# Optimization experiments

Hardware: AMD Instinct MI355X
Metric: run time of the kernel (lower is better)

Reference implementation:

```python
import jax, jax.numpy as jnp
import numpy as np
jax.config.update("jax_enable_x64", True)  # hashing uses int64 primes as in torch

N_PTS = 1048576
L, T, F = 16, 2 ** 18, 2
N_MIN, N_MAX = 16, 1024
HID, OUT = 64, 3


def setup_inputs() -> dict:
    key = jax.random.key(0)
    ks = jax.random.split(key, 6)
    X = jax.random.uniform(ks[0], (N_PTS, 2), dtype=jnp.float32)
    hash_table = jax.random.uniform(ks[1], (L, T, F), dtype=jnp.float32,
                                    minval=-1e-4, maxval=1e-4)
    def lin(k, fan_in, fan_out):
        bound = 1.0 / np.sqrt(fan_in)
        kw, kb = jax.random.split(k)
        W = jax.random.uniform(kw, (fan_in, fan_out), dtype=jnp.float32,
                               minval=-bound, maxval=bound)
        b = jax.random.uniform(kb, (fan_out,), dtype=jnp.float32,
                               minval=-bound, maxval=bound)
        return W, b
    W1, b1 = lin(ks[2], L * F, HID)
    W2, b2 = lin(ks[3], HID, HID)
    W3, b3 = lin(ks[4], HID, HID)
    W4, b4 = lin(ks[5], HID, OUT)
    return {"X": X, "hash_table": hash_table,
            "W1": W1, "b1": b1, "W2": W2, "b2": b2,
            "W3": W3, "b3": b3, "W4": W4, "b4": b4}


def reference(X, hash_table, W1, b1, W2, b2, W3, b3, W4, b4):
    Lh, Th, Fh = hash_table.shape
    # per-level resolutions: floor(N_min * b**l), b geometric between N_min and N_max
    b_geo = np.exp((np.log(N_MAX) - np.log(N_MIN)) / (Lh - 1))
    N_values = jnp.floor(jnp.asarray(N_MIN * b_geo ** np.arange(Lh),
                                     dtype=jnp.float32))  # (L,)

    x_scaled = X[:, :, None] * N_values[None, None, :]        # (N, 2, L)
    x_floor = jnp.floor(x_scaled)

    # NOTE: original code MULTIPLIES floor coords by the 0/1 vertex pattern
    # (not add) -- we replicate that math faithfully.
    vertices = jnp.array([[0., 0., 1., 1.], [0., 1., 0., 1.]],
                         dtype=jnp.float32)                   # (2, 4)
    x_vert = (x_floor[:, :, :, None] * vertices[None, :, None, :]
              ).astype(jnp.int64)                             # (N, 2, L, 4)

    primes = jnp.array([1, 2654435761], dtype=jnp.int64)
    hv = x_vert * primes[None, :, None, None]
    x_hash = jnp.remainder(jnp.bitwise_xor(hv[:, 0], hv[:, 1]), Th)  # (N, L, 4)

    # irregular gather: per-level hash table lookup -> (N, L, 4, F)
    lookup = hash_table[jnp.arange(Lh)[None, :, None], x_hash]

    w = x_scaled - x_floor                                    # (N, 2, L)
    fx, fy = w[:, 0, :], w[:, 1, :]
    cx, cy = 1.0 - fx, 1.0 - fy
    f_stack = jnp.stack([cx * cy, cx * fy, fx * cy, fx * fy], axis=2)  # (N, L, 4)

    x_interp = jnp.sum(f_stack[:, :, :, None] * lookup, axis=2)  # (N, L, F)
    feat = x_interp.reshape(-1, Lh * Fh).astype(jnp.float32)     # (N, 32)

    h = jax.nn.leaky_relu(feat @ W1 + b1)
    h = jax.nn.leaky_relu(h @ W2 + b2)
    h = jax.nn.leaky_relu(h @ W3 + b3)
    return jax.nn.relu(h @ W4 + b4)
```

## Files before the change

kernel.cpp:

```cpp
#include <hip/hip_runtime.h>
#include <math.h>

typedef _Float16 half8  __attribute__((ext_vector_type(8)));
typedef float    float4v __attribute__((ext_vector_type(4)));

constexpr int T_ = 1 << 18;
constexpr unsigned TMASK = T_ - 1;
constexpr unsigned PRIME = 2654435761u;

constexpr int WFRAG_HALFS = 22 * 64 * 8;
constexpr int BIAS_FLOATS = 208;
constexpr int WS_BYTES    = 22528 + 240 * 4;
constexpr int WS_UINT4    = WS_BYTES / 16;
constexpr int V12_OFF     = 23488;

constexpr int BLK   = 256;
constexpr int PTS_PER_BLOCK = 512;

struct Meta { float n[16]; float off[16]; };

__global__ void prep_weights(const float* __restrict__ W1, const float* __restrict__ b1,
                             const float* __restrict__ W2, const float* __restrict__ b2,
                             const float* __restrict__ W3, const float* __restrict__ b3,
                             const float* __restrict__ W4, const float* __restrict__ b4,
                             const float2* __restrict__ table,
                             _Float16* __restrict__ wsW, float* __restrict__ wsB,
                             uint2* __restrict__ wsV, Meta mv)
{
    const int tid = threadIdx.x;
    const int bid = blockIdx.x;
    if (bid < 44) {
        const int e = bid * 256 + tid;
        const int frag = e >> 9;
        const int l    = (e >> 3) & 63;
        const int j    = e & 7;
        const int g = l >> 4, m = l & 15;
        const int u = j >> 2, r = j & 3;
        float v;
        if (frag < 4) {
            v = W1[(8*g + j) * 64 + 16*frag + m];
        } else if (frag < 12) {
            const int s = (frag - 4) >> 2, t = (frag - 4) & 3;
            v = W2[(32*s + 16*u + 4*g + r) * 64 + 16*t + m];
        } else if (frag < 20) {
            const int s = (frag - 12) >> 2, t = (frag - 12) & 3;
            v = W3[(32*s + 16*u + 4*g + r) * 64 + 16*t + m];
        } else {
            const int s = frag - 20;
            v = (m < 3) ? W4[(32*s + 16*u + 4*g + r) * 3 + m] : 0.f;
        }
        wsW[e] = (_Float16)v;
    } else if (bid == 44) {
        if (tid < 64) { wsB[tid] = b1[tid]; wsB[64 + tid] = b2[tid]; wsB[128 + tid] = b3[tid]; }
        else if (tid < 80)  { const int r2 = tid - 64; wsB[192 + r2] = (r2 < 3) ? b4[r2] : 0.f; }
        else if (tid < 96)  wsB[BIAS_FLOATS + (tid - 80)] = mv.n[tid - 80];
        else if (tid < 112) wsB[BIAS_FLOATS + 16 + (tid - 96)] = mv.off[tid - 96];
    } else {
        const int e = (bid - 45) * 256 + tid;
        const int total = (int)mv.off[15] + (int)mv.n[15] + 1;
        if (e < total) {
            int l = 0;
            #pragma unroll
            for (int k = 1; k < 16; ++k) if (e >= (int)mv.off[k]) l = k;
            const int i = e - (int)mv.off[l];
            const float2* tl = table + (size_t)l * T_;
            const float2 b = tl[((unsigned)i * PRIME) & TMASK];
            const float2 a = tl[i];
            union { _Float16 h[2]; unsigned u; } p0, p1;
            p0.h[0] = (_Float16)b.x; p0.h[1] = (_Float16)b.y;
            p1.h[0] = (_Float16)a.x; p1.h[1] = (_Float16)a.y;
            wsV[e] = uint2{p0.u, p1.u};
        }
    }
}

struct Gather {
    float2   v3[4];
    unsigned v1[4];
    unsigned v2[4];
};

__device__ __forceinline__ void issue_gather(Gather& G, const float2 xy,
                                             const float2* __restrict__ table,
                                             const unsigned* __restrict__ gV12,
                                             const float (&nvq)[4], const int (&offq)[4],
                                             const int g)
{
    #pragma unroll
    for (int q = 0; q < 4; ++q) {
        const float n = nvq[q];
        const float xs = xy.x * n, ys = xy.y * n;
        const int xi = (int)floorf(xs);
        const int yi = (int)floorf(ys);
        const unsigned yp = (unsigned)yi * PRIME;
        G.v3[q] = table[(size_t)(4*g + q) * T_ + (((unsigned)xi ^ yp) & TMASK)];
        G.v1[q] = gV12[2*(offq[q] + yi) + 0];
        G.v2[q] = gV12[2*(offq[q] + xi) + 1];
    }
}

__device__ __forceinline__ half8 make_feat(const float2 xy, const Gather& G,
                                           const float (&nvq)[4],
                                           const float2 (&v0c)[4])
{
    half8 feat;
    #pragma unroll
    for (int q = 0; q < 4; ++q) {
        const float n = nvq[q];
        const float xs = xy.x * n, ys = xy.y * n;
        const float xf = floorf(xs), yf = floorf(ys);
        const float fx = xs - xf, fy = ys - yf;
        union { unsigned u; _Float16 h[2]; } u1, u2;
        u1.u = G.v1[q]; u2.u = G.v2[q];
        const float cx = 1.f - fx, cy = 1.f - fy;
        const float w0 = cx*cy, w1 = cx*fy, w2 = fx*cy, w3 = fx*fy;
        feat[2*q+0] = (_Float16)(w0*v0c[q].x + w1*(float)u1.h[0] + w2*(float)u2.h[0] + w3*G.v3[q].x);
        feat[2*q+1] = (_Float16)(w0*v0c[q].y + w1*(float)u1.h[1] + w2*(float)u2.h[1] + w3*G.v3[q].y);
    }
    return feat;
}

__device__ __forceinline__ void repack(const float4v (&acc)[4], half8& a0, half8& a1)
{
    #pragma unroll
    for (int u = 0; u < 2; ++u)
        #pragma unroll
        for (int r = 0; r < 4; ++r) {
            const float v0 = acc[u][r];
            const float v1 = acc[2 + u][r];
            a0[4*u + r] = (_Float16)(v0 > 0.f ? v0 : 0.01f * v0);
            a1[4*u + r] = (_Float16)(v1 > 0.f ? v1 : 0.01f * v1);
        }
}

__global__ __launch_bounds__(BLK)
void fused_hashnerf_mfma(const float2* __restrict__ X,
                         const float2* __restrict__ table,
                         const uint4* __restrict__ ws,
                         float* __restrict__ out)
{
    __shared__ uint4 sRaw[WS_UINT4];

    const int tid = threadIdx.x;
    for (int i = tid; i < WS_UINT4; i += BLK) sRaw[i] = ws[i];
    __syncthreads();

    const _Float16* Wl = (const _Float16*)sRaw;
    const float*    Bl = (const float*)(sRaw + (22528 / 16));
    const unsigned* gV12 = (const unsigned*)((const char*)ws + V12_OFF);

    const int wave = tid >> 6, lane = tid & 63;
    const int g = lane >> 4, c = lane & 15;

    float4v b1f[4], b2f[4], b3f[4], b4f;
    #pragma unroll
    for (int t = 0; t < 4; ++t) {
        b1f[t] = *(const float4v*)(Bl +       16*t + 4*g);
        b2f[t] = *(const float4v*)(Bl +  64 + 16*t + 4*g);
        b3f[t] = *(const float4v*)(Bl + 128 + 16*t + 4*g);
    }
    b4f = *(const float4v*)(Bl + 192 + 4*g);
    float nvq[4];
    int   offq[4];
    #pragma unroll
    for (int q = 0; q < 4; ++q) {
        nvq[q]  = Bl[BIAS_FLOATS + 4*g + q];
        offq[q] = (int)Bl[BIAS_FLOATS + 16 + 4*g + q];
    }

    const int base_pt = blockIdx.x * PTS_PER_BLOCK + wave * 128;

    float2 xy[8];
    #pragma unroll
    for (int it = 0; it < 8; ++it) xy[it] = X[base_pt + it*16 + c];

    float2 v0c[4];
    #pragma unroll
    for (int q = 0; q < 4; ++q) v0c[q] = table[(size_t)(4*g + q) * T_];

    Gather G0, G1, G2;
    issue_gather(G0, xy[0], table, gV12, nvq, offq, g);
    issue_gather(G1, xy[1], table, gV12, nvq, offq, g);

    #pragma unroll
    for (int it = 0; it < 8; ++it) {
        Gather& Gc = (it % 3 == 0) ? G0 : (it % 3 == 1) ? G1 : G2;
        Gather& Gn = ((it + 2) % 3 == 0) ? G0 : ((it + 2) % 3 == 1) ? G1 : G2;

        const half8 feat = make_feat(xy[it], Gc, nvq, v0c);

        if (it < 6) issue_gather(Gn, xy[it+2], table, gV12, nvq, offq, g);
        __builtin_amdgcn_sched_barrier(0);

        float4v acc[4];
        #pragma unroll
        for (int t = 0; t < 4; ++t) {
            const half8 wf = *(const half8*)(Wl + (t*64 + lane)*8);
            acc[t] = __builtin_amdgcn_mfma_f32_16x16x32_f16(wf, feat, b1f[t], 0, 0, 0);
        }

        half8 a0, a1;
        repack(acc, a0, a1);
        #pragma unroll
        for (int t = 0; t < 4; ++t) {
            const half8 w0f = *(const half8*)(Wl + ((4 + t)*64 + lane)*8);
            const half8 w1f = *(const half8*)(Wl + ((8 + t)*64 + lane)*8);
            float4v a = __builtin_amdgcn_mfma_f32_16x16x32_f16(w0f, a0, b2f[t], 0, 0, 0);
            acc[t]    = __builtin_amdgcn_mfma_f32_16x16x32_f16(w1f, a1, a,      0, 0, 0);
        }

        repack(acc, a0, a1);
        #pragma unroll
        for (int t = 0; t < 4; ++t) {
            const half8 w0f = *(const half8*)(Wl + ((12 + t)*64 + lane)*8);
            const half8 w1f = *(const half8*)(Wl + ((16 + t)*64 + lane)*8);
            float4v a = __builtin_amdgcn_mfma_f32_16x16x32_f16(w0f, a0, b3f[t], 0, 0, 0);
            acc[t]    = __builtin_amdgcn_mfma_f32_16x16x32_f16(w1f, a1, a,      0, 0, 0);
        }

        repack(acc, a0, a1);
        const half8 w40 = *(const half8*)(Wl + (20*64 + lane)*8);
        const half8 w41 = *(const half8*)(Wl + (21*64 + lane)*8);
        float4v o = __builtin_amdgcn_mfma_f32_16x16x32_f16(w40, a0, b4f, 0, 0, 0);
        o         = __builtin_amdgcn_mfma_f32_16x16x32_f16(w41, a1, o,   0, 0, 0);
        if (g == 0) {
            float* op = out + (size_t)3 * (base_pt + it * 16 + c);
            op[0] = fmaxf(o[0], 0.f);
            op[1] = fmaxf(o[1], 0.f);
            op[2] = fmaxf(o[2], 0.f);
        }
    }
}

extern "C" void kernel_launch(void* const* d_in, const int* in_sizes, int n_in,
                              void* d_out, int out_size, void* d_ws, size_t ws_size,
                              hipStream_t stream) {
    const float2* X     = (const float2*)d_in[0];
    const float2* table = (const float2*)d_in[1];
    const float*  W1    = (const float*)d_in[2];
    const float*  b1    = (const float*)d_in[3];
    const float*  W2    = (const float*)d_in[4];
    const float*  b2    = (const float*)d_in[5];
    const float*  W3    = (const float*)d_in[6];
    const float*  b3    = (const float*)d_in[7];
    const float*  W4    = (const float*)d_in[8];
    const float*  b4    = (const float*)d_in[9];
    float* out          = (float*)d_out;

    const int npts = in_sizes[0] / 2;

    Meta mv;
    const double bg = exp((log(1024.0) - log(16.0)) / 15.0);
    int acc = 0;
    for (int l = 0; l < 16; ++l) {
        const float nl = floorf((float)(16.0 * pow(bg, (double)l)));
        mv.n[l]   = nl;
        mv.off[l] = (float)acc;
        acc += (int)nl + 1;
    }

    _Float16* wsW = (_Float16*)d_ws;
    float*    wsB = (float*)((char*)d_ws + 22528);
    uint2*    wsV = (uint2*)((char*)d_ws + V12_OFF);

    prep_weights<<<62, 256, 0, stream>>>(W1, b1, W2, b2, W3, b3, W4, b4, table,
                                         wsW, wsB, wsV, mv);
    fused_hashnerf_mfma<<<npts / PTS_PER_BLOCK, BLK, 0, stream>>>(X, table, (const uint4*)d_ws, out);
}
```

Before: 222.5 us.

## Precompute fp16 per-cell corner table for low-resolution levels in workspace

Adds a prep kernel that builds a compact fp16 table holding the (x,y) corner value for every grid cell of levels 0-12, indexed densely as yi*(n+1)+xi. The top three levels keep their hashed indexing but are copied to fp16. The main kernel then gathers the fourth corner from this smaller, denser, half-width table instead of the full fp32 hash table, which should improve cache locality and cut gather bytes. The fractional weights are now computed once at issue time and carried in registers. In exchange there is an extra prep pass over several MB every call, more workspace, a fallback path when the workspace is too small, and extra register pressure.

```diff
diff --git a/kernel.cpp b/kernel.cpp
--- a/kernel.cpp
+++ b/kernel.cpp
@@ -10,14 +10,15 @@
 
 constexpr int WFRAG_HALFS = 22 * 64 * 8;
 constexpr int BIAS_FLOATS = 208;
-constexpr int WS_BYTES    = 22528 + 240 * 4;
+constexpr int WS_BYTES    = 22528 + 256 * 4;
 constexpr int WS_UINT4    = WS_BYTES / 16;
-constexpr int V12_OFF     = 23488;
+constexpr int V12_OFF     = 23552;
+constexpr int TC_OFF      = 57344;
 
 constexpr int BLK   = 256;
 constexpr int PTS_PER_BLOCK = 512;
 
-struct Meta { float n[16]; float off[16]; };
+struct Meta { float n[16]; float off[16]; float cb[16]; };
 
 __global__ void prep_weights(const float* __restrict__ W1, const float* __restrict__ b1,
                              const float* __restrict__ W2, const float* __restrict__ b2,
@@ -53,8 +54,9 @@
     } else if (bid == 44) {
         if (tid < 64) { wsB[tid] = b1[tid]; wsB[64 + tid] = b2[tid]; wsB[128 + tid] = b3[tid]; }
         else if (tid < 80)  { const int r2 = tid - 64; wsB[192 + r2] = (r2 < 3) ? b4[r2] : 0.f; }
-        else if (tid < 96)  wsB[BIAS_FLOATS + (tid - 80)] = mv.n[tid - 80];
+        else if (tid < 96)  wsB[BIAS_FLOATS +      (tid - 80)] = mv.n[tid - 80];
         else if (tid < 112) wsB[BIAS_FLOATS + 16 + (tid - 96)] = mv.off[tid - 96];
+        else if (tid < 128) wsB[BIAS_FLOATS + 32 + (tid - 112)] = mv.cb[tid - 112];
     } else {
         const int e = (bid - 45) * 256 + tid;
         const int total = (int)mv.off[15] + (int)mv.n[15] + 1;
@@ -74,48 +76,82 @@
     }
 }
 
+__global__ void prep_tc(const float2* __restrict__ table, unsigned* __restrict__ tc,
+                        Meta mv, int total)
+{
+    const int e = blockIdx.x * 256 + threadIdx.x;
+    if (e >= total) return;
+    int l = 0;
+    #pragma unroll
+    for (int k = 1; k < 16; ++k) if (e >= (int)mv.cb[k]) l = k;
+    const int rel = e - (int)mv.cb[l];
+    unsigned src;
+    if (l <= 12) {
+        const int p  = (int)mv.n[l] + 1;
+        const int yi = rel / p, xi = rel - yi * p;
+        src = ((unsigned)xi ^ ((unsigned)yi * PRIME)) & TMASK;
+    } else {
+        src = (unsigned)rel;
+    }
+    const float2 v = table[(size_t)l * T_ + src];
+    union { _Float16 h[2]; unsigned u; } pk;
+    pk.h[0] = (_Float16)v.x; pk.h[1] = (_Float16)v.y;
+    tc[e] = pk.u;
+}
+
 struct Gather {
-    float2   v3[4];
-    unsigned v1[4];
-    unsigned v2[4];
+    float    fx[4], fy[4];
+    unsigned v3u[4];
+    float2   v3f[4];
+    unsigned v1[4], v2[4];
 };
 
+template<int MODE>
 __device__ __forceinline__ void issue_gather(Gather& G, const float2 xy,
                                              const float2* __restrict__ table,
+                                             const unsigned* __restrict__ tc,
                                              const unsigned* __restrict__ gV12,
                                              const float (&nvq)[4], const int (&offq)[4],
+                                             const unsigned (&cbq)[4], const int (&pq)[4],
                                              const int g)
 {
-    #pragma unroll
-    for (int q = 0; q < 4; ++q) {
-        const float n = nvq[q];
-        const float xs = xy.x * n, ys = xy.y * n;
-        const int xi = (int)floorf(xs);
-        const int yi = (int)floorf(ys);
-        const unsigned yp = (unsigned)yi * PRIME;
-        G.v3[q] = table[(size_t)(4*g + q) * T_ + (((unsigned)xi ^ yp) & TMASK)];
-        G.v1[q] = gV12[2*(offq[q] + yi) + 0];
-        G.v2[q] = gV12[2*(offq[q] + xi) + 1];
-    }
-}
-
-__device__ __forceinline__ half8 make_feat(const float2 xy, const Gather& G,
-                                           const float (&nvq)[4],
-                                           const float2 (&v0c)[4])
-{
-    half8 feat;
     #pragma unroll
     for (int q = 0; q < 4; ++q) {
         const float n = nvq[q];
         const float xs = xy.x * n, ys = xy.y * n;
         const float xf = floorf(xs), yf = floorf(ys);
-        const float fx = xs - xf, fy = ys - yf;
-        union { unsigned u; _Float16 h[2]; } u1, u2;
+        G.fx[q] = xs - xf; G.fy[q] = ys - yf;
+        const int xi = (int)xf, yi = (int)yf;
+        if constexpr (MODE == 3) {
+            unsigned idx;
+            if (q == 0 || g < 3) idx = cbq[q] + (unsigned)(yi * pq[q] + xi);
+            else                 idx = cbq[q] + (((unsigned)xi ^ ((unsigned)yi * PRIME)) & TMASK);
+            G.v3u[q] = tc[idx];
+        } else {
+            const unsigned yp = (unsigned)yi * PRIME;
+            G.v3f[q] = table[(size_t)(4*g + q) * T_ + (((unsigned)xi ^ yp) & TMASK)];
+        }
+        G.v1[q] = gV12[2*(offq[q] + yi) + 0];
+        G.v2[q] = gV12[2*(offq[q] + xi) + 1];
+    }
+}
+
+template<int MODE>
+__device__ __forceinline__ half8 make_feat(const Gather& G, const float2 (&v0c)[4])
+{
+    half8 feat;
+    #pragma unroll
+    for (int q = 0; q < 4; ++q) {
+        const float fx = G.fx[q], fy = G.fy[q];
+        union { unsigned u; _Float16 h[2]; } u1, u2, u3;
         u1.u = G.v1[q]; u2.u = G.v2[q];
+        float v3x, v3y;
+        if constexpr (MODE == 3) { u3.u = G.v3u[q]; v3x = (float)u3.h[0]; v3y = (float)u3.h[1]; }
+        else                     { v3x = G.v3f[q].x; v3y = G.v3f[q].y; }
         const float cx = 1.f - fx, cy = 1.f - fy;
         const float w0 = cx*cy, w1 = cx*fy, w2 = fx*cy, w3 = fx*fy;
-        feat[2*q+0] = (_Float16)(w0*v0c[q].x + w1*(float)u1.h[0] + w2*(float)u2.h[0] + w3*G.v3[q].x);
-        feat[2*q+1] = (_Float16)(w0*v0c[q].y + w1*(float)u1.h[1] + w2*(float)u2.h[1] + w3*G.v3[q].y);
+        feat[2*q+0] = (_Float16)(w0*v0c[q].x + w1*(float)u1.h[0] + w2*(float)u2.h[0] + w3*v3x);
+        feat[2*q+1] = (_Float16)(w0*v0c[q].y + w1*(float)u1.h[1] + w2*(float)u2.h[1] + w3*v3y);
     }
     return feat;
 }
@@ -133,6 +169,7 @@
         }
 }
 
+template<int MODE>
 __global__ __launch_bounds__(BLK)
 void fused_hashnerf_mfma(const float2* __restrict__ X,
                          const float2* __restrict__ table,
@@ -148,6 +185,7 @@
     const _Float16* Wl = (const _Float16*)sRaw;
     const float*    Bl = (const float*)(sRaw + (22528 / 16));
     const unsigned* gV12 = (const unsigned*)((const char*)ws + V12_OFF);
+    const unsigned* tc   = (const unsigned*)((const char*)ws + TC_OFF);
 
     const int wave = tid >> 6, lane = tid & 63;
     const int g = lane >> 4, c = lane & 15;
@@ -160,12 +198,16 @@
         b3f[t] = *(const float4v*)(Bl + 128 + 16*t + 4*g);
     }
     b4f = *(const float4v*)(Bl + 192 + 4*g);
-    float nvq[4];
-    int   offq[4];
+    float    nvq[4];
+    int      offq[4];
+    unsigned cbq[4];
+    int      pq[4];
     #pragma unroll
     for (int q = 0; q < 4; ++q) {
-        nvq[q]  = Bl[BIAS_FLOATS + 4*g + q];
+        nvq[q]  = Bl[BIAS_FLOATS +      4*g + q];
         offq[q] = (int)Bl[BIAS_FLOATS + 16 + 4*g + q];
+        cbq[q]  = (unsigned)Bl[BIAS_FLOATS + 32 + 4*g + q];
+        pq[q]   = (int)nvq[q] + 1;
     }
 
     const int base_pt = blockIdx.x * PTS_PER_BLOCK + wave * 128;
@@ -179,17 +221,17 @@
     for (int q = 0; q < 4; ++q) v0c[q] = table[(size_t)(4*g + q) * T_];
 
     Gather G0, G1, G2;
-    issue_gather(G0, xy[0], table, gV12, nvq, offq, g);
-    issue_gather(G1, xy[1], table, gV12, nvq, offq, g);
+    issue_gather<MODE>(G0, xy[0], table, tc, gV12, nvq, offq, cbq, pq, g);
+    issue_gather<MODE>(G1, xy[1], table, tc, gV12, nvq, offq, cbq, pq, g);
 
     #pragma unroll
     for (int it = 0; it < 8; ++it) {
         Gather& Gc = (it % 3 == 0) ? G0 : (it % 3 == 1) ? G1 : G2;
         Gather& Gn = ((it + 2) % 3 == 0) ? G0 : ((it + 2) % 3 == 1) ? G1 : G2;
 
-        const half8 feat = make_feat(xy[it], Gc, nvq, v0c);
-
-        if (it < 6) issue_gather(Gn, xy[it+2], table, gV12, nvq, offq, g);
+        const half8 feat = make_feat<MODE>(Gc, v0c);
+
+        if (it < 6) issue_gather<MODE>(Gn, xy[it+2], table, tc, gV12, nvq, offq, cbq, pq, g);
         __builtin_amdgcn_sched_barrier(0);
 
         float4v acc[4];
@@ -258,12 +300,28 @@
         mv.off[l] = (float)acc;
         acc += (int)nl + 1;
     }
+    unsigned cbacc = 0;
+    for (int l = 0; l < 16; ++l) {
+        mv.cb[l] = (float)cbacc;
+        const int p = (int)mv.n[l] + 1;
+        cbacc += (l <= 12) ? (unsigned)(p * p) : (unsigned)T_;
+    }
+    const unsigned total_tc = cbacc;
 
     _Float16* wsW = (_Float16*)d_ws;
     float*    wsB = (float*)((char*)d_ws + 22528);
     uint2*    wsV = (uint2*)((char*)d_ws + V12_OFF);
+    unsigned* tc  = (unsigned*)((char*)d_ws + TC_OFF);
+
+    const int grid = npts / PTS_PER_BLOCK;
 
     prep_weights<<<62, 256, 0, stream>>>(W1, b1, W2, b2, W3, b3, W4, b4, table,
                                          wsW, wsB, wsV, mv);
-    fused_hashnerf_mfma<<<npts / PTS_PER_BLOCK, BLK, 0, stream>>>(X, table, (const uint4*)d_ws, out);
-}
+
+    if (ws_size >= (size_t)TC_OFF + (size_t)total_tc * 4) {
+        prep_tc<<<(int)((total_tc + 255) / 256), 256, 0, stream>>>(table, tc, mv, (int)total_tc);
+        fused_hashnerf_mfma<3><<<grid, BLK, 0, stream>>>(X, table, (const uint4*)d_ws, out);
+    } else {
+        fused_hashnerf_mfma<0><<<grid, BLK, 0, stream>>>(X, table, (const uint4*)d_ws, out);
+    }
+}
```

New measurement: 208.9 us. 1.07x faster.
